# Performance work log

Hardware: AMD Instinct MI355X
Metric: run time of the kernel (lower is better)

The kernel has to match this reference:

```python
import jax, jax.numpy as jnp
import numpy as np

BETA = 1000.0   # partial_ot default beta
N_ITER = 10     # partial_ot default n_iter


def setup_inputs() -> dict:
    key = jax.random.key(0)
    k1, k2 = jax.random.split(key)
    v_emb = jax.random.normal(k1, (64, 512, 256), dtype=jnp.float32)
    a_emb = jax.random.normal(k2, (64, 512, 256), dtype=jnp.float32)
    return {"v_emb": v_emb, "a_emb": a_emb}


def reference(v_emb, a_emb):
    # calc_pot_loss of UMT with p=2: cost_routines[2](x, y) = cdist(x, y)**2 / 2.
    B, m, d = v_emb.shape
    n = a_emb.shape[1]
    # Batched squared-Euclidean cost / 2 -> [B, m, n]
    C = 0.5 * (jnp.sum(v_emb * v_emb, -1)[:, :, None]
               + jnp.sum(a_emb * a_emb, -1)[:, None, :]
               - 2.0 * jnp.einsum('bmd,bnd->bmn', v_emb, a_emb))
    T0 = jnp.exp(-C / BETA)                       # Gibbs kernel, [B, m, n]
    S0 = jnp.sum(T0, axis=(-2, -1))               # total mass, [B]
    rs0 = jnp.sum(T0[:, 0, :], axis=-1)           # row-0 sum, [B]
    cs0 = jnp.sum(T0[:, :, 0], axis=-1)           # col-0 sum, [B]

    # Literal torch semantics of partial_ot:
    #  - torch.diag(k) on the [m,1] / [n,1] vectors returns a length-1 tensor
    #    (the diagonal of an m-by-1 matrix), so T_a / T_b are SCALAR rescalings
    #    of T by min(a[0]/rowsum[0], 1) and min(b[0]/colsum[0], 1).
    #  - D is reset to +inf at the top of every s-iteration, so the returned D
    #    is exactly the value computed at the last s = min(m, n).
    # Hence every T in the s/t loops is c * T0 for a per-batch scalar c, and we
    # track only that scalar recurrence (same math, no redundant matrices).
    a0 = 1.0 / m                                  # a = ones(m,1)/m -> a[0]
    b0 = 1.0 / n                                  # b = ones(n,1)/n -> b[0]
    s = float(min(m, n))                          # only last s survives

    c = s / S0                                    # T = (s / sum(T)) * exp(-C/beta)
    for _ in range(N_ITER):
        k_a = jnp.minimum(a0 / (c * rs0), 1.0)            # diag(min(a/T@1, 1))[0]
        k_b = jnp.minimum(b0 / (k_a * c * cs0), 1.0)      # diag(min(b/T_a.T@1, 1))[0]
        c = s * k_a * k_b / S0                            # T = (s/sum(T_old)) * T_b

    D = c * jnp.einsum('bmn,bmn->b', C, T0)       # dot(C.flatten(), T.flatten())
    return jnp.mean(D)                            # mean over batch (stacked distances)
```

## Files before the change

### kernel.cpp

```cpp
#include <hip/hip_runtime.h>
#include <stdint.h>

#define BATCH 64
#define MDIM 512
#define NDIM 512
#define KDIM 256
#define BM 128
#define BN 128
#define BK 32
#define NKSTEP 8
#define NTILES 16
#define LDSW 32

typedef __attribute__((ext_vector_type(8))) short short8;
typedef __attribute__((ext_vector_type(4))) float f32x4;
typedef __attribute__((ext_vector_type(4))) unsigned int u32x4;

__device__ __forceinline__ unsigned int cvt_pk(float lo, float hi) {
  unsigned int r;
  asm("v_cvt_pk_bf16_f32 %0, %1, %2" : "=v"(r) : "v"(lo), "v"(hi));
  return r;
}

#define BARRIER()                                         \
  {                                                       \
    asm volatile("s_waitcnt lgkmcnt(0)" ::: "memory");    \
    __builtin_amdgcn_s_barrier();                         \
    asm volatile("" ::: "memory");                        \
  }

__device__ __forceinline__ float waveRedSum(float v) {
  v += __shfl_xor(v, 32);
  v += __shfl_xor(v, 16);
  v += __shfl_xor(v, 8);
  v += __shfl_xor(v, 4);
  v += __shfl_xor(v, 2);
  v += __shfl_xor(v, 1);
  return v;
}

__global__ __launch_bounds__(512, 4) void pot_gemm_reduce(
    const float* __restrict__ V, const float* __restrict__ A,
    float* __restrict__ part) {
  const int bid = blockIdx.x;
  const int lin = (bid & 7) * 128 + (bid >> 3);
  const int b   = lin >> 4;
  const int t   = lin & 15;
  const int tm  = t >> 2;
  const int tn  = t & 3;

  const int tid  = threadIdx.x;
  const int w    = tid >> 6;
  const int lane = tid & 63;
  const int wr   = w >> 2;
  const int wc   = w & 3;
  const int srow = tid >> 2;
  const int sseg = tid & 3;
  const int ssw  = (sseg ^ ((srow >> 1) & 3)) * 8;

  __shared__ short As[2][BM][LDSW];
  __shared__ short Bs[2][BN][LDSW];
  __shared__ float nvs[BM];
  __shared__ float nas[BN];
  __shared__ float red[8][4];

  const float* Vg = V + ((size_t)b * MDIM + (size_t)tm * BM + srow) * KDIM + sseg * 8;
  const float* Ag = A + ((size_t)b * NDIM + (size_t)tn * BN + srow) * KDIM + sseg * 8;

  float sqa = 0.f, sqb = 0.f;
  f32x4 acc[4][2];
#pragma unroll
  for (int m = 0; m < 4; ++m)
#pragma unroll
    for (int n = 0; n < 2; ++n)
      acc[m][n] = (f32x4){0.f, 0.f, 0.f, 0.f};

  float4 ra[2][2], rb[2][2];

#define ISSUE(k, slot)                                                        \
  {                                                                           \
    const float4* pa = reinterpret_cast<const float4*>(Vg + (k) * BK);        \
    const float4* pb = reinterpret_cast<const float4*>(Ag + (k) * BK);        \
    ra[slot][0] = pa[0]; ra[slot][1] = pa[1];                                 \
    rb[slot][0] = pb[0]; rb[slot][1] = pb[1];                                 \
  }

#define SQ4(s_, f) { s_ += (f).x*(f).x + (f).y*(f).y + (f).z*(f).z + (f).w*(f).w; }

#define WRITE(buf, slot)                                                      \
  {                                                                           \
    u32x4 wa, wb;                                                             \
    wa[0] = cvt_pk(ra[slot][0].x, ra[slot][0].y);                             \
    wa[1] = cvt_pk(ra[slot][0].z, ra[slot][0].w);                             \
    wa[2] = cvt_pk(ra[slot][1].x, ra[slot][1].y);                             \
    wa[3] = cvt_pk(ra[slot][1].z, ra[slot][1].w);                             \
    wb[0] = cvt_pk(rb[slot][0].x, rb[slot][0].y);                             \
    wb[1] = cvt_pk(rb[slot][0].z, rb[slot][0].w);                             \
    wb[2] = cvt_pk(rb[slot][1].x, rb[slot][1].y);                             \
    wb[3] = cvt_pk(rb[slot][1].z, rb[slot][1].w);                             \
    SQ4(sqa, ra[slot][0]); SQ4(sqa, ra[slot][1]);                             \
    SQ4(sqb, rb[slot][0]); SQ4(sqb, rb[slot][1]);                             \
    *reinterpret_cast<u32x4*>(&As[buf][srow][ssw]) = wa;                      \
    *reinterpret_cast<u32x4*>(&Bs[buf][srow][ssw]) = wb;                      \
  }

#define COMPUTE(buf)                                                          \
  {                                                                           \
    short8 af[4], bf[2];                                                      \
    const int fr  = lane & 15;                                                \
    const int ksw = ((lane >> 4) ^ ((fr >> 1) & 3)) * 8;   \
    _Pragma("unroll")                                                         \
    for (int m = 0; m < 4; ++m)                                               \
      af[m] = *reinterpret_cast<const short8*>(                               \
          &As[buf][wr * 64 + m * 16 + fr][ksw]);                              \
    _Pragma("unroll")                                                         \
    for (int n = 0; n < 2; ++n)                                               \
      bf[n] = *reinterpret_cast<const short8*>(                               \
          &Bs[buf][wc * 32 + n * 16 + fr][ksw]);                              \
    _Pragma("unroll")                                                         \
    for (int m = 0; m < 4; ++m)                                               \
      _Pragma("unroll")                                                       \
      for (int n = 0; n < 2; ++n)                                             \
        acc[m][n] = __builtin_amdgcn_mfma_f32_16x16x32_bf16(                  \
            af[m], bf[n], acc[m][n], 0, 0, 0);                                \
  }

  ISSUE(0, 0);
  ISSUE(1, 1);
  WRITE(0, 0);
  BARRIER();

#pragma unroll
  for (int k = 0; k < NKSTEP; ++k) {
    if (k + 2 < NKSTEP) ISSUE(k + 2, k & 1);
    COMPUTE(k & 1);
    if (k + 1 < NKSTEP) WRITE((k + 1) & 1, (k + 1) & 1);
    BARRIER();
  }

  {
    float va = sqa;
    va += __shfl_xor(va, 1); va += __shfl_xor(va, 2);
    float vb = sqb;
    vb += __shfl_xor(vb, 1); vb += __shfl_xor(vb, 2);
    if (sseg == 0) { nvs[srow] = 0.5f * va; nas[srow] = 0.5f * vb; }
  }
  BARRIER();

  float hr[4][4], hc[2];
#pragma unroll
  for (int m = 0; m < 4; ++m)
#pragma unroll
    for (int r = 0; r < 4; ++r)
      hr[m][r] = nvs[wr * 64 + m * 16 + (lane >> 4) * 4 + r];
#pragma unroll
  for (int n = 0; n < 2; ++n)
    hc[n] = nas[wc * 32 + n * 16 + (lane & 15)];

  const bool rowmask = (tm == 0) && (wr == 0) && ((lane >> 4) == 0);
  const bool colmask = (tn == 0) && (wc == 0) && ((lane & 15) == 0);
  const float k2 = -1.0e-3f * 1.4426950408889634f;

  float s0p = 0.f, ctp = 0.f, rsp = 0.f, csp = 0.f;
#pragma unroll
  for (int m = 0; m < 4; ++m) {
#pragma unroll
    for (int n = 0; n < 2; ++n) {
#pragma unroll
      for (int r = 0; r < 4; ++r) {
        float Cv = hr[m][r] + hc[n] - acc[m][n][r];
        float T = exp2f(Cv * k2);
        s0p += T;
        ctp += Cv * T;
        if (m == 0 && r == 0) rsp += rowmask ? T : 0.f;
        if (n == 0)           csp += colmask ? T : 0.f;
      }
    }
  }

  s0p = waveRedSum(s0p);
  ctp = waveRedSum(ctp);
  rsp = waveRedSum(rsp);
  csp = waveRedSum(csp);
  if (lane == 0) { red[w][0] = s0p; red[w][1] = ctp; red[w][2] = rsp; red[w][3] = csp; }
  BARRIER();
  if (tid == 0) {
    float s0 = 0.f, ct = 0.f, rs = 0.f, cs = 0.f;
#pragma unroll
    for (int i = 0; i < 8; ++i) {
      s0 += red[i][0]; ct += red[i][1]; rs += red[i][2]; cs += red[i][3];
    }
    float* p = part + ((size_t)(b * NTILES + t)) * 4;
    p[0] = s0; p[1] = ct; p[2] = rs; p[3] = cs;
  }
}

__global__ __launch_bounds__(64) void pot_finalize(
    const float* __restrict__ part, float* __restrict__ out) {
  const int b = threadIdx.x;
  float S0 = 0.f, CT = 0.f, RS = 0.f, CS = 0.f;
#pragma unroll
  for (int t = 0; t < NTILES; ++t) {
    const float* p = part + ((size_t)(b * NTILES + t)) * 4;
    S0 += p[0]; CT += p[1]; RS += p[2]; CS += p[3];
  }
  const float a0 = 1.0f / (float)MDIM;
  const float b0 = 1.0f / (float)NDIM;
  const float s  = (float)MDIM;
  float c = s / S0;
#pragma unroll
  for (int i = 0; i < 10; ++i) {
    float ka = fminf(a0 / (c * RS), 1.0f);
    float kb = fminf(b0 / (ka * c * CS), 1.0f);
    c = s * ka * kb / S0;
  }
  float D = c * CT;
  D = waveRedSum(D);
  if (b == 0) out[0] = D * (1.0f / (float)BATCH);
}

extern "C" void kernel_launch(void* const* d_in, const int* in_sizes, int n_in,
                              void* d_out, int out_size, void* d_ws, size_t ws_size,
                              hipStream_t stream) {
  const float* V = (const float*)d_in[0];
  const float* A = (const float*)d_in[1];
  float* out = (float*)d_out;
  float* part = (float*)d_ws;

  pot_gemm_reduce<<<dim3(BATCH * NTILES), 512, 0, stream>>>(V, A, part);
  pot_finalize<<<1, 64, 0, stream>>>(part, out);
}
```

Baseline: 29.96 us.

## Keep V row-tile in registers and stream all A column tiles per block

Each block now owns one 128-row V tile for one batch, loads its full K=256 slice once into LDS and then into register fragments, and loops over the four A column tiles. It double-buffers those A tiles through LDS, prefetching and converting the next tile while running MFMAs on the current one. The grid shrinks from 1024 to 256 blocks, and V is loaded and converted once instead of four times. Per-wave partials are written directly to global memory instead of being reduced in-block, so the finalize kernel reads 8x more partials. The cost is a large register footprint (afr holds 32 short8), occupancy lowered to 2 blocks per CU in the launch bounds, and a smaller grid.

```diff
diff --git a/kernel.cpp b/kernel.cpp
--- a/kernel.cpp
+++ b/kernel.cpp
@@ -3,14 +3,10 @@
 
 #define BATCH 64
 #define MDIM 512
-#define NDIM 512
 #define KDIM 256
-#define BM 128
-#define BN 128
-#define BK 32
-#define NKSTEP 8
-#define NTILES 16
-#define LDSW 32
+#define BT   128
+#define NTN  4
+#define NBLK 256
 
 typedef __attribute__((ext_vector_type(8))) short short8;
 typedef __attribute__((ext_vector_type(4))) float f32x4;
@@ -28,6 +24,8 @@
     __builtin_amdgcn_s_barrier();                         \
     asm volatile("" ::: "memory");                        \
   }
+
+#define SQ4(s_, f) { s_ += (f).x*(f).x + (f).y*(f).y + (f).z*(f).z + (f).w*(f).w; }
 
 __device__ __forceinline__ float waveRedSum(float v) {
   v += __shfl_xor(v, 32);
@@ -39,15 +37,13 @@
   return v;
 }
 
-__global__ __launch_bounds__(512, 4) void pot_gemm_reduce(
-    const float* __restrict__ V, const float* __restrict__ A,
+__global__ __launch_bounds__(512, 2) void pot_fused(
+    const float* __restrict__ V, const float* __restrict__ Ae,
     float* __restrict__ part) {
-  const int bid = blockIdx.x;
-  const int lin = (bid & 7) * 128 + (bid >> 3);
-  const int b   = lin >> 4;
-  const int t   = lin & 15;
-  const int tm  = t >> 2;
-  const int tn  = t & 3;
+  const int pid = blockIdx.x;
+  const int L   = (pid & 7) * 32 + (pid >> 3);
+  const int b   = L >> 2;
+  const int tm  = L & 3;
 
   const int tid  = threadIdx.x;
   const int w    = tid >> 6;
@@ -56,142 +52,200 @@
   const int wc   = w & 3;
   const int srow = tid >> 2;
   const int sseg = tid & 3;
-  const int ssw  = (sseg ^ ((srow >> 1) & 3)) * 8;
-
-  __shared__ short As[2][BM][LDSW];
-  __shared__ short Bs[2][BN][LDSW];
-  __shared__ float nvs[BM];
-  __shared__ float nas[BN];
-  __shared__ float red[8][4];
-
-  const float* Vg = V + ((size_t)b * MDIM + (size_t)tm * BM + srow) * KDIM + sseg * 8;
-  const float* Ag = A + ((size_t)b * NDIM + (size_t)tn * BN + srow) * KDIM + sseg * 8;
-
-  float sqa = 0.f, sqb = 0.f;
-  f32x4 acc[4][2];
-#pragma unroll
-  for (int m = 0; m < 4; ++m)
-#pragma unroll
-    for (int n = 0; n < 2; ++n)
-      acc[m][n] = (f32x4){0.f, 0.f, 0.f, 0.f};
-
-  float4 ra[2][2], rb[2][2];
-
-#define ISSUE(k, slot)                                                        \
-  {                                                                           \
-    const float4* pa = reinterpret_cast<const float4*>(Vg + (k) * BK);        \
-    const float4* pb = reinterpret_cast<const float4*>(Ag + (k) * BK);        \
-    ra[slot][0] = pa[0]; ra[slot][1] = pa[1];                                 \
-    rb[slot][0] = pb[0]; rb[slot][1] = pb[1];                                 \
-  }
-
-#define SQ4(s_, f) { s_ += (f).x*(f).x + (f).y*(f).y + (f).z*(f).z + (f).w*(f).w; }
-
-#define WRITE(buf, slot)                                                      \
-  {                                                                           \
-    u32x4 wa, wb;                                                             \
-    wa[0] = cvt_pk(ra[slot][0].x, ra[slot][0].y);                             \
-    wa[1] = cvt_pk(ra[slot][0].z, ra[slot][0].w);                             \
-    wa[2] = cvt_pk(ra[slot][1].x, ra[slot][1].y);                             \
-    wa[3] = cvt_pk(ra[slot][1].z, ra[slot][1].w);                             \
-    wb[0] = cvt_pk(rb[slot][0].x, rb[slot][0].y);                             \
-    wb[1] = cvt_pk(rb[slot][0].z, rb[slot][0].w);                             \
-    wb[2] = cvt_pk(rb[slot][1].x, rb[slot][1].y);                             \
-    wb[3] = cvt_pk(rb[slot][1].z, rb[slot][1].w);                             \
-    SQ4(sqa, ra[slot][0]); SQ4(sqa, ra[slot][1]);                             \
-    SQ4(sqb, rb[slot][0]); SQ4(sqb, rb[slot][1]);                             \
-    *reinterpret_cast<u32x4*>(&As[buf][srow][ssw]) = wa;                      \
-    *reinterpret_cast<u32x4*>(&Bs[buf][srow][ssw]) = wb;                      \
-  }
-
-#define COMPUTE(buf)                                                          \
-  {                                                                           \
-    short8 af[4], bf[2];                                                      \
-    const int fr  = lane & 15;                                                \
-    const int ksw = ((lane >> 4) ^ ((fr >> 1) & 3)) * 8;   \
-    _Pragma("unroll")                                                         \
-    for (int m = 0; m < 4; ++m)                                               \
-      af[m] = *reinterpret_cast<const short8*>(                               \
-          &As[buf][wr * 64 + m * 16 + fr][ksw]);                              \
-    _Pragma("unroll")                                                         \
-    for (int n = 0; n < 2; ++n)                                               \
-      bf[n] = *reinterpret_cast<const short8*>(                               \
-          &Bs[buf][wc * 32 + n * 16 + fr][ksw]);                              \
-    _Pragma("unroll")                                                         \
-    for (int m = 0; m < 4; ++m)                                               \
-      _Pragma("unroll")                                                       \
-      for (int n = 0; n < 2; ++n)                                             \
-        acc[m][n] = __builtin_amdgcn_mfma_f32_16x16x32_bf16(                  \
-            af[m], bf[n], acc[m][n], 0, 0, 0);                                \
-  }
-
-  ISSUE(0, 0);
-  ISSUE(1, 1);
-  WRITE(0, 0);
+  const int fr   = lane & 15;
+  const int fk   = lane >> 4;
+
+  __shared__ short buf[2][BT][KDIM];
+  __shared__ float nvs[BT];
+  __shared__ float nbs[2][BT];
+
+  const float* Arow = V  + ((size_t)b * MDIM + tm * BT + srow) * KDIM;
+  const float* Brow = Ae + ((size_t)b * MDIM + srow) * KDIM;
+
+  {
+    float4 st[16];
+#pragma unroll
+    for (int i = 0; i < 8; ++i) {
+      const float4* p = reinterpret_cast<const float4*>(Arow + (sseg + 4 * i) * 8);
+      st[2 * i] = p[0]; st[2 * i + 1] = p[1];
+    }
+    float sq = 0.f;
+#pragma unroll
+    for (int i = 0; i < 8; ++i) {
+      const int u = (sseg + 4 * i) ^ (srow & 7);
+      u32x4 wv;
+      wv[0] = cvt_pk(st[2 * i].x, st[2 * i].y);
+      wv[1] = cvt_pk(st[2 * i].z, st[2 * i].w);
+      wv[2] = cvt_pk(st[2 * i + 1].x, st[2 * i + 1].y);
+      wv[3] = cvt_pk(st[2 * i + 1].z, st[2 * i + 1].w);
+      SQ4(sq, st[2 * i]); SQ4(sq, st[2 * i + 1]);
+      *reinterpret_cast<u32x4*>(&buf[1][srow][u * 8]) = wv;
+    }
+    sq += __shfl_xor(sq, 1); sq += __shfl_xor(sq, 2);
+    if (sseg == 0) nvs[srow] = 0.5f * sq;
+  }
+
+  float4 b0st[16];
+#pragma unroll
+  for (int i = 0; i < 8; ++i) {
+    const float4* p = reinterpret_cast<const float4*>(Brow + (sseg + 4 * i) * 8);
+    b0st[2 * i] = p[0]; b0st[2 * i + 1] = p[1];
+  }
   BARRIER();
 
-#pragma unroll
-  for (int k = 0; k < NKSTEP; ++k) {
-    if (k + 2 < NKSTEP) ISSUE(k + 2, k & 1);
-    COMPUTE(k & 1);
-    if (k + 1 < NKSTEP) WRITE((k + 1) & 1, (k + 1) & 1);
+  {
+    float sq = 0.f;
+#pragma unroll
+    for (int i = 0; i < 8; ++i) {
+      const int u = (sseg + 4 * i) ^ (srow & 7);
+      u32x4 wv;
+      wv[0] = cvt_pk(b0st[2 * i].x, b0st[2 * i].y);
+      wv[1] = cvt_pk(b0st[2 * i].z, b0st[2 * i].w);
+      wv[2] = cvt_pk(b0st[2 * i + 1].x, b0st[2 * i + 1].y);
+      wv[3] = cvt_pk(b0st[2 * i + 1].z, b0st[2 * i + 1].w);
+      SQ4(sq, b0st[2 * i]); SQ4(sq, b0st[2 * i + 1]);
+      *reinterpret_cast<u32x4*>(&buf[0][srow][u * 8]) = wv;
+    }
+    sq += __shfl_xor(sq, 1); sq += __shfl_xor(sq, 2);
+    if (sseg == 0) nbs[0][srow] = 0.5f * sq;
+  }
+
+  short8 afr[4][8];
+#pragma unroll
+  for (int m = 0; m < 4; ++m) {
+#pragma unroll
+    for (int ks = 0; ks < 8; ++ks) {
+      const int row = wr * 64 + m * 16 + fr;
+      const int u   = (4 * ks + fk) ^ (row & 7);
+      afr[m][ks] = *reinterpret_cast<const short8*>(&buf[1][row][u * 8]);
+    }
+  }
+  BARRIER();
+
+  const float k2 = -1.0e-3f * 1.4426950408889634f;
+  float4 bst[2][4];
+
+#pragma unroll
+  for (int tn = 0; tn < NTN; ++tn) {
+    const int bb = tn & 1;
+    const int nb = bb ^ 1;
+    const float* Bnx = Brow + (size_t)(tn + 1) * BT * KDIM;
+
+    f32x4 acc[4][2];
+#pragma unroll
+    for (int m = 0; m < 4; ++m)
+#pragma unroll
+      for (int n = 0; n < 2; ++n)
+        acc[m][n] = (f32x4){0.f, 0.f, 0.f, 0.f};
+
+#define BISSUE(i0, slot)                                                       \
+    {                                                                          \
+      const float4* p0_ = reinterpret_cast<const float4*>(Bnx + (sseg + 4*(i0)) * 8);     \
+      const float4* p1_ = reinterpret_cast<const float4*>(Bnx + (sseg + 4*((i0)+1)) * 8); \
+      bst[slot][0] = p0_[0]; bst[slot][1] = p0_[1];                            \
+      bst[slot][2] = p1_[0]; bst[slot][3] = p1_[1];                            \
+    }
+#define BWRITE(i0, slot)                                                       \
+    {                                                                          \
+      int u_ = (sseg + 4*(i0)) ^ (srow & 7);                                   \
+      u32x4 wv_;                                                               \
+      wv_[0] = cvt_pk(bst[slot][0].x, bst[slot][0].y);                         \
+      wv_[1] = cvt_pk(bst[slot][0].z, bst[slot][0].w);                         \
+      wv_[2] = cvt_pk(bst[slot][1].x, bst[slot][1].y);                         \
+      wv_[3] = cvt_pk(bst[slot][1].z, bst[slot][1].w);                         \
+      SQ4(sqb, bst[slot][0]); SQ4(sqb, bst[slot][1]);                          \
+      *reinterpret_cast<u32x4*>(&buf[nb][srow][u_ * 8]) = wv_;                 \
+      u_ = (sseg + 4*((i0)+1)) ^ (srow & 7);                                   \
+      wv_[0] = cvt_pk(bst[slot][2].x, bst[slot][2].y);                         \
+      wv_[1] = cvt_pk(bst[slot][2].z, bst[slot][2].w);                         \
+      wv_[2] = cvt_pk(bst[slot][3].x, bst[slot][3].y);                         \
+      wv_[3] = cvt_pk(bst[slot][3].z, bst[slot][3].w);                         \
+      SQ4(sqb, bst[slot][2]); SQ4(sqb, bst[slot][3]);                          \
+      *reinterpret_cast<u32x4*>(&buf[nb][srow][u_ * 8]) = wv_;                 \
+    }
+
+    float sqb = 0.f;
+    short8 bfr[2][2];
+#pragma unroll
+    for (int n = 0; n < 2; ++n) {
+      const int row = wc * 32 + n * 16 + fr;
+      const int u   = fk ^ (row & 7);
+      bfr[0][n] = *reinterpret_cast<const short8*>(&buf[bb][row][u * 8]);
+    }
+
+#pragma unroll
+    for (int ks = 0; ks < 8; ++ks) {
+      if (ks < 7) {
+#pragma unroll
+        for (int n = 0; n < 2; ++n) {
+          const int row = wc * 32 + n * 16 + fr;
+          const int u   = (4 * (ks + 1) + fk) ^ (row & 7);
+          bfr[(ks + 1) & 1][n] =
+              *reinterpret_cast<const short8*>(&buf[bb][row][u * 8]);
+        }
+      }
+      if (tn < NTN - 1) {
+        if (ks == 0) { BISSUE(0, 0); }
+        if (ks == 2) { BWRITE(0, 0); BISSUE(2, 1); }
+        if (ks == 4) { BWRITE(2, 1); BISSUE(4, 0); }
+        if (ks == 6) { BWRITE(4, 0); BISSUE(6, 1); }
+      }
+#pragma unroll
+      for (int m = 0; m < 4; ++m)
+#pragma unroll
+        for (int n = 0; n < 2; ++n)
+          acc[m][n] = __builtin_amdgcn_mfma_f32_16x16x32_bf16(
+              afr[m][ks], bfr[ks & 1][n], acc[m][n], 0, 0, 0);
+    }
+
+    if (tn < NTN - 1) {
+      BWRITE(6, 1);
+      sqb += __shfl_xor(sqb, 1); sqb += __shfl_xor(sqb, 2);
+      if (sseg == 0) nbs[nb][srow] = 0.5f * sqb;
+    }
+
+    {
+      float hr[4][4], hc[2];
+#pragma unroll
+      for (int m = 0; m < 4; ++m)
+#pragma unroll
+        for (int r = 0; r < 4; ++r)
+          hr[m][r] = nvs[wr * 64 + m * 16 + fk * 4 + r];
+#pragma unroll
+      for (int n = 0; n < 2; ++n)
+        hc[n] = nbs[bb][wc * 32 + n * 16 + fr];
+
+      const bool rowmask = (tm == 0) && (wr == 0) && (fk == 0);
+      const bool colmask = (tn == 0) && (wc == 0) && (fr == 0);
+
+      float s0p = 0.f, ctp = 0.f, rsp = 0.f, csp = 0.f;
+#pragma unroll
+      for (int m = 0; m < 4; ++m) {
+#pragma unroll
+        for (int n = 0; n < 2; ++n) {
+#pragma unroll
+          for (int r = 0; r < 4; ++r) {
+            float Cv = hr[m][r] + hc[n] - acc[m][n][r];
+            float T = exp2f(Cv * k2);
+            s0p += T;
+            ctp += Cv * T;
+            if (m == 0 && r == 0) rsp += rowmask ? T : 0.f;
+            if (n == 0)           csp += colmask ? T : 0.f;
+          }
+        }
+      }
+      s0p = waveRedSum(s0p);
+      ctp = waveRedSum(ctp);
+      rsp = waveRedSum(rsp);
+      csp = waveRedSum(csp);
+      if (lane == 0) {
+        float* p = part + (((size_t)(L * NTN + tn)) * 8 + w) * 4;
+        p[0] = s0p; p[1] = ctp; p[2] = rsp; p[3] = csp;
+      }
+    }
     BARRIER();
-  }
-
-  {
-    float va = sqa;
-    va += __shfl_xor(va, 1); va += __shfl_xor(va, 2);
-    float vb = sqb;
-    vb += __shfl_xor(vb, 1); vb += __shfl_xor(vb, 2);
-    if (sseg == 0) { nvs[srow] = 0.5f * va; nas[srow] = 0.5f * vb; }
-  }
-  BARRIER();
-
-  float hr[4][4], hc[2];
-#pragma unroll
-  for (int m = 0; m < 4; ++m)
-#pragma unroll
-    for (int r = 0; r < 4; ++r)
-      hr[m][r] = nvs[wr * 64 + m * 16 + (lane >> 4) * 4 + r];
-#pragma unroll
-  for (int n = 0; n < 2; ++n)
-    hc[n] = nas[wc * 32 + n * 16 + (lane & 15)];
-
-  const bool rowmask = (tm == 0) && (wr == 0) && ((lane >> 4) == 0);
-  const bool colmask = (tn == 0) && (wc == 0) && ((lane & 15) == 0);
-  const float k2 = -1.0e-3f * 1.4426950408889634f;
-
-  float s0p = 0.f, ctp = 0.f, rsp = 0.f, csp = 0.f;
-#pragma unroll
-  for (int m = 0; m < 4; ++m) {
-#pragma unroll
-    for (int n = 0; n < 2; ++n) {
-#pragma unroll
-      for (int r = 0; r < 4; ++r) {
-        float Cv = hr[m][r] + hc[n] - acc[m][n][r];
-        float T = exp2f(Cv * k2);
-        s0p += T;
-        ctp += Cv * T;
-        if (m == 0 && r == 0) rsp += rowmask ? T : 0.f;
-        if (n == 0)           csp += colmask ? T : 0.f;
-      }
-    }
-  }
-
-  s0p = waveRedSum(s0p);
-  ctp = waveRedSum(ctp);
-  rsp = waveRedSum(rsp);
-  csp = waveRedSum(csp);
-  if (lane == 0) { red[w][0] = s0p; red[w][1] = ctp; red[w][2] = rsp; red[w][3] = csp; }
-  BARRIER();
-  if (tid == 0) {
-    float s0 = 0.f, ct = 0.f, rs = 0.f, cs = 0.f;
-#pragma unroll
-    for (int i = 0; i < 8; ++i) {
-      s0 += red[i][0]; ct += red[i][1]; rs += red[i][2]; cs += red[i][3];
-    }
-    float* p = part + ((size_t)(b * NTILES + t)) * 4;
-    p[0] = s0; p[1] = ct; p[2] = rs; p[3] = cs;
+#undef BISSUE
+#undef BWRITE
   }
 }
 
@@ -200,12 +254,18 @@
   const int b = threadIdx.x;
   float S0 = 0.f, CT = 0.f, RS = 0.f, CS = 0.f;
 #pragma unroll
-  for (int t = 0; t < NTILES; ++t) {
-    const float* p = part + ((size_t)(b * NTILES + t)) * 4;
-    S0 += p[0]; CT += p[1]; RS += p[2]; CS += p[3];
+  for (int tm = 0; tm < 4; ++tm) {
+    const int L = 4 * b + tm;
+#pragma unroll
+    for (int tn = 0; tn < NTN; ++tn) {
+      for (int wv = 0; wv < 8; ++wv) {
+        const float* p = part + (((size_t)(L * NTN + tn)) * 8 + wv) * 4;
+        S0 += p[0]; CT += p[1]; RS += p[2]; CS += p[3];
+      }
+    }
   }
   const float a0 = 1.0f / (float)MDIM;
-  const float b0 = 1.0f / (float)NDIM;
+  const float b0 = 1.0f / (float)MDIM;
   const float s  = (float)MDIM;
   float c = s / S0;
 #pragma unroll
@@ -222,11 +282,11 @@
 extern "C" void kernel_launch(void* const* d_in, const int* in_sizes, int n_in,
                               void* d_out, int out_size, void* d_ws, size_t ws_size,
                               hipStream_t stream) {
-  const float* V = (const float*)d_in[0];
-  const float* A = (const float*)d_in[1];
-  float* out = (float*)d_out;
+  const float* V  = (const float*)d_in[0];
+  const float* Ae = (const float*)d_in[1];
+  float* out  = (float*)d_out;
   float* part = (float*)d_ws;
 
-  pot_gemm_reduce<<<dim3(BATCH * NTILES), 512, 0, stream>>>(V, A, part);
+  pot_fused<<<dim3(NBLK), 512, 0, stream>>>(V, Ae, part);
   pot_finalize<<<1, 64, 0, stream>>>(part, out);
 }
```

New measurement: 36.74 us. 22.6% more time.

## Restructure GEMM tiles: full-K A strip in LDS, B fed straight from registers

Applied to the files above, without the earlier changes.

Each block now loads a 64-row strip of V with the full K depth into LDS once and computes 64x256 output tiles. Each wave streams its own 32 columns of A from global memory straight into MFMA B-operand registers, with no LDS staging or per-step barriers. Per-wave partial sums are written directly, which removes the block-level reduction, and the finalize kernel is widened to 256 threads. The aim is to cut barrier and LDS traffic and raise occupancy. The cost is no software prefetch on the global loads for A and more partials to reduce at the end.

```diff
diff --git a/kernel.cpp b/kernel.cpp
--- a/kernel.cpp
+++ b/kernel.cpp
@@ -3,14 +3,10 @@
 
 #define BATCH 64
 #define MDIM 512
-#define NDIM 512
 #define KDIM 256
-#define BM 128
-#define BN 128
-#define BK 32
-#define NKSTEP 8
-#define NTILES 16
-#define LDSW 32
+#define ROWS 64
+#define HCOLS 256
+#define NBLK 1024
 
 typedef __attribute__((ext_vector_type(8))) short short8;
 typedef __attribute__((ext_vector_type(4))) float f32x4;
@@ -21,13 +17,6 @@
   asm("v_cvt_pk_bf16_f32 %0, %1, %2" : "=v"(r) : "v"(lo), "v"(hi));
   return r;
 }
-
-#define BARRIER()                                         \
-  {                                                       \
-    asm volatile("s_waitcnt lgkmcnt(0)" ::: "memory");    \
-    __builtin_amdgcn_s_barrier();                         \
-    asm volatile("" ::: "memory");                        \
-  }
 
 __device__ __forceinline__ float waveRedSum(float v) {
   v += __shfl_xor(v, 32);
@@ -39,126 +28,109 @@
   return v;
 }
 
-__global__ __launch_bounds__(512, 4) void pot_gemm_reduce(
-    const float* __restrict__ V, const float* __restrict__ A,
+__global__ __launch_bounds__(512, 8) void pot_gemm_reduce(
+    const float* __restrict__ V, const float* __restrict__ Ae,
     float* __restrict__ part) {
   const int bid = blockIdx.x;
   const int lin = (bid & 7) * 128 + (bid >> 3);
-  const int b   = lin >> 4;
-  const int t   = lin & 15;
-  const int tm  = t >> 2;
-  const int tn  = t & 3;
+  const int b     = lin >> 4;
+  const int strip = (lin >> 1) & 7;
+  const int half  = lin & 1;
 
   const int tid  = threadIdx.x;
   const int w    = tid >> 6;
   const int lane = tid & 63;
-  const int wr   = w >> 2;
-  const int wc   = w & 3;
-  const int srow = tid >> 2;
-  const int sseg = tid & 3;
-  const int ssw  = (sseg ^ ((srow >> 1) & 3)) * 8;
-
-  __shared__ short As[2][BM][LDSW];
-  __shared__ short Bs[2][BN][LDSW];
-  __shared__ float nvs[BM];
-  __shared__ float nas[BN];
-  __shared__ float red[8][4];
-
-  const float* Vg = V + ((size_t)b * MDIM + (size_t)tm * BM + srow) * KDIM + sseg * 8;
-  const float* Ag = A + ((size_t)b * NDIM + (size_t)tn * BN + srow) * KDIM + sseg * 8;
-
-  float sqa = 0.f, sqb = 0.f;
+  const int fr   = lane & 15;
+  const int fk   = lane >> 4;
+  const int frl  = fr & 7;
+
+  __shared__ short As[ROWS][KDIM];
+  __shared__ float nvs[ROWS];
+
+  {
+    const int row = tid >> 3;
+    const int j   = tid & 7;
+    const float* Ar = V + ((size_t)b * MDIM + strip * ROWS + row) * KDIM;
+    float sq = 0.f;
+#pragma unroll
+    for (int i = 0; i < 4; ++i) {
+      const int u = j * 4 + i;
+      const float4* p = reinterpret_cast<const float4*>(Ar + u * 8);
+      float4 x = p[0], y = p[1];
+      u32x4 wv;
+      wv[0] = cvt_pk(x.x, x.y); wv[1] = cvt_pk(x.z, x.w);
+      wv[2] = cvt_pk(y.x, y.y); wv[3] = cvt_pk(y.z, y.w);
+      sq += x.x * x.x + x.y * x.y + x.z * x.z + x.w * x.w;
+      sq += y.x * y.x + y.y * y.y + y.z * y.z + y.w * y.w;
+      *reinterpret_cast<u32x4*>(&As[row][(u ^ (row & 7)) * 8]) = wv;
+    }
+    sq += __shfl_xor(sq, 1);
+    sq += __shfl_xor(sq, 2);
+    sq += __shfl_xor(sq, 4);
+    if (j == 0) nvs[row] = 0.5f * sq;
+  }
+  __syncthreads();
+
+  const int gcb = half * HCOLS + w * 32;
+  const float* B0 = Ae + ((size_t)b * MDIM + gcb + fr) * KDIM + fk * 8;
+  const float* B1 = B0 + 16 * KDIM;
+
   f32x4 acc[4][2];
 #pragma unroll
   for (int m = 0; m < 4; ++m)
 #pragma unroll
     for (int n = 0; n < 2; ++n)
       acc[m][n] = (f32x4){0.f, 0.f, 0.f, 0.f};
-
-  float4 ra[2][2], rb[2][2];
-
-#define ISSUE(k, slot)                                                        \
-  {                                                                           \
-    const float4* pa = reinterpret_cast<const float4*>(Vg + (k) * BK);        \
-    const float4* pb = reinterpret_cast<const float4*>(Ag + (k) * BK);        \
-    ra[slot][0] = pa[0]; ra[slot][1] = pa[1];                                 \
-    rb[slot][0] = pb[0]; rb[slot][1] = pb[1];                                 \
-  }
-
-#define SQ4(s_, f) { s_ += (f).x*(f).x + (f).y*(f).y + (f).z*(f).z + (f).w*(f).w; }
-
-#define WRITE(buf, slot)                                                      \
-  {                                                                           \
-    u32x4 wa, wb;                                                             \
-    wa[0] = cvt_pk(ra[slot][0].x, ra[slot][0].y);                             \
-    wa[1] = cvt_pk(ra[slot][0].z, ra[slot][0].w);                             \
-    wa[2] = cvt_pk(ra[slot][1].x, ra[slot][1].y);                             \
-    wa[3] = cvt_pk(ra[slot][1].z, ra[slot][1].w);                             \
-    wb[0] = cvt_pk(rb[slot][0].x, rb[slot][0].y);                             \
-    wb[1] = cvt_pk(rb[slot][0].z, rb[slot][0].w);                             \
-    wb[2] = cvt_pk(rb[slot][1].x, rb[slot][1].y);                             \
-    wb[3] = cvt_pk(rb[slot][1].z, rb[slot][1].w);                             \
-    SQ4(sqa, ra[slot][0]); SQ4(sqa, ra[slot][1]);                             \
-    SQ4(sqb, rb[slot][0]); SQ4(sqb, rb[slot][1]);                             \
-    *reinterpret_cast<u32x4*>(&As[buf][srow][ssw]) = wa;                      \
-    *reinterpret_cast<u32x4*>(&Bs[buf][srow][ssw]) = wb;                      \
-  }
-
-#define COMPUTE(buf)                                                          \
-  {                                                                           \
-    short8 af[4], bf[2];                                                      \
-    const int fr  = lane & 15;                                                \
-    const int ksw = ((lane >> 4) ^ ((fr >> 1) & 3)) * 8;   \
-    _Pragma("unroll")                                                         \
-    for (int m = 0; m < 4; ++m)                                               \
-      af[m] = *reinterpret_cast<const short8*>(                               \
-          &As[buf][wr * 64 + m * 16 + fr][ksw]);                              \
-    _Pragma("unroll")                                                         \
-    for (int n = 0; n < 2; ++n)                                               \
-      bf[n] = *reinterpret_cast<const short8*>(                               \
-          &Bs[buf][wc * 32 + n * 16 + fr][ksw]);                              \
-    _Pragma("unroll")                                                         \
-    for (int m = 0; m < 4; ++m)                                               \
-      _Pragma("unroll")                                                       \
-      for (int n = 0; n < 2; ++n)                                             \
-        acc[m][n] = __builtin_amdgcn_mfma_f32_16x16x32_bf16(                  \
-            af[m], bf[n], acc[m][n], 0, 0, 0);                                \
-  }
-
-  ISSUE(0, 0);
-  ISSUE(1, 1);
-  WRITE(0, 0);
-  BARRIER();
-
-#pragma unroll
-  for (int k = 0; k < NKSTEP; ++k) {
-    if (k + 2 < NKSTEP) ISSUE(k + 2, k & 1);
-    COMPUTE(k & 1);
-    if (k + 1 < NKSTEP) WRITE((k + 1) & 1, (k + 1) & 1);
-    BARRIER();
-  }
-
-  {
-    float va = sqa;
-    va += __shfl_xor(va, 1); va += __shfl_xor(va, 2);
-    float vb = sqb;
-    vb += __shfl_xor(vb, 1); vb += __shfl_xor(vb, 2);
-    if (sseg == 0) { nvs[srow] = 0.5f * va; nas[srow] = 0.5f * vb; }
-  }
-  BARRIER();
-
-  float hr[4][4], hc[2];
+  float sqb0 = 0.f, sqb1 = 0.f;
+
+#pragma unroll
+  for (int ks = 0; ks < 8; ++ks) {
+    float4 x0 = *reinterpret_cast<const float4*>(B0 + ks * 32);
+    float4 x1 = *reinterpret_cast<const float4*>(B0 + ks * 32 + 4);
+    float4 y0 = *reinterpret_cast<const float4*>(B1 + ks * 32);
+    float4 y1 = *reinterpret_cast<const float4*>(B1 + ks * 32 + 4);
+    u32x4 t0, t1;
+    t0[0] = cvt_pk(x0.x, x0.y); t0[1] = cvt_pk(x0.z, x0.w);
+    t0[2] = cvt_pk(x1.x, x1.y); t0[3] = cvt_pk(x1.z, x1.w);
+    t1[0] = cvt_pk(y0.x, y0.y); t1[1] = cvt_pk(y0.z, y0.w);
+    t1[2] = cvt_pk(y1.x, y1.y); t1[3] = cvt_pk(y1.z, y1.w);
+    sqb0 += x0.x * x0.x + x0.y * x0.y + x0.z * x0.z + x0.w * x0.w;
+    sqb0 += x1.x * x1.x + x1.y * x1.y + x1.z * x1.z + x1.w * x1.w;
+    sqb1 += y0.x * y0.x + y0.y * y0.y + y0.z * y0.z + y0.w * y0.w;
+    sqb1 += y1.x * y1.x + y1.y * y1.y + y1.z * y1.z + y1.w * y1.w;
+    short8 bf0 = *reinterpret_cast<short8*>(&t0);
+    short8 bf1 = *reinterpret_cast<short8*>(&t1);
+
+    const int su = ((4 * ks + fk) ^ frl) * 8;
+    short8 af0 = *reinterpret_cast<const short8*>(&As[fr][su]);
+    short8 af1 = *reinterpret_cast<const short8*>(&As[16 + fr][su]);
+    short8 af2 = *reinterpret_cast<const short8*>(&As[32 + fr][su]);
+    short8 af3 = *reinterpret_cast<const short8*>(&As[48 + fr][su]);
+
+    acc[0][0] = __builtin_amdgcn_mfma_f32_16x16x32_bf16(af0, bf0, acc[0][0], 0, 0, 0);
+    acc[0][1] = __builtin_amdgcn_mfma_f32_16x16x32_bf16(af0, bf1, acc[0][1], 0, 0, 0);
+    acc[1][0] = __builtin_amdgcn_mfma_f32_16x16x32_bf16(af1, bf0, acc[1][0], 0, 0, 0);
+    acc[1][1] = __builtin_amdgcn_mfma_f32_16x16x32_bf16(af1, bf1, acc[1][1], 0, 0, 0);
+    acc[2][0] = __builtin_amdgcn_mfma_f32_16x16x32_bf16(af2, bf0, acc[2][0], 0, 0, 0);
+    acc[2][1] = __builtin_amdgcn_mfma_f32_16x16x32_bf16(af2, bf1, acc[2][1], 0, 0, 0);
+    acc[3][0] = __builtin_amdgcn_mfma_f32_16x16x32_bf16(af3, bf0, acc[3][0], 0, 0, 0);
+    acc[3][1] = __builtin_amdgcn_mfma_f32_16x16x32_bf16(af3, bf1, acc[3][1], 0, 0, 0);
+  }
+
+  sqb0 += __shfl_xor(sqb0, 16); sqb0 += __shfl_xor(sqb0, 32);
+  sqb1 += __shfl_xor(sqb1, 16); sqb1 += __shfl_xor(sqb1, 32);
+  const float hc0 = 0.5f * sqb0;
+  const float hc1 = 0.5f * sqb1;
+
+  float hr[4][4];
 #pragma unroll
   for (int m = 0; m < 4; ++m)
 #pragma unroll
     for (int r = 0; r < 4; ++r)
-      hr[m][r] = nvs[wr * 64 + m * 16 + (lane >> 4) * 4 + r];
-#pragma unroll
-  for (int n = 0; n < 2; ++n)
-    hc[n] = nas[wc * 32 + n * 16 + (lane & 15)];
-
-  const bool rowmask = (tm == 0) && (wr == 0) && ((lane >> 4) == 0);
-  const bool colmask = (tn == 0) && (wc == 0) && ((lane & 15) == 0);
+      hr[m][r] = nvs[m * 16 + fk * 4 + r];
+
+  const bool rowmask = (strip == 0) && (fk == 0);
+  const bool colmask = (half == 0) && (w == 0) && (fr == 0);
   const float k2 = -1.0e-3f * 1.4426950408889634f;
 
   float s0p = 0.f, ctp = 0.f, rsp = 0.f, csp = 0.f;
@@ -168,7 +140,7 @@
     for (int n = 0; n < 2; ++n) {
 #pragma unroll
       for (int r = 0; r < 4; ++r) {
-        float Cv = hr[m][r] + hc[n] - acc[m][n][r];
+        float Cv = hr[m][r] + (n ? hc1 : hc0) - acc[m][n][r];
         float T = exp2f(Cv * k2);
         s0p += T;
         ctp += Cv * T;
@@ -182,51 +154,59 @@
   ctp = waveRedSum(ctp);
   rsp = waveRedSum(rsp);
   csp = waveRedSum(csp);
-  if (lane == 0) { red[w][0] = s0p; red[w][1] = ctp; red[w][2] = rsp; red[w][3] = csp; }
-  BARRIER();
-  if (tid == 0) {
-    float s0 = 0.f, ct = 0.f, rs = 0.f, cs = 0.f;
-#pragma unroll
-    for (int i = 0; i < 8; ++i) {
-      s0 += red[i][0]; ct += red[i][1]; rs += red[i][2]; cs += red[i][3];
+  if (lane == 0) {
+    float* p = part + (((size_t)((b * 16 + strip * 2 + half)) * 8 + w)) * 4;
+    p[0] = s0p; p[1] = ctp; p[2] = rsp; p[3] = csp;
+  }
+}
+
+__global__ __launch_bounds__(256) void pot_finalize(
+    const float* __restrict__ part, float* __restrict__ out) {
+  __shared__ float dred[BATCH];
+  const int t = threadIdx.x;
+  const int batch = t >> 2;
+  const int q = t & 3;
+
+  float S0 = 0.f, CT = 0.f, RS = 0.f, CS = 0.f;
+  const f32x4* p4 = reinterpret_cast<const f32x4*>(part);
+#pragma unroll
+  for (int i = 0; i < 32; ++i) {
+    f32x4 v = p4[batch * 128 + q * 32 + i];
+    S0 += v[0]; CT += v[1]; RS += v[2]; CS += v[3];
+  }
+  S0 += __shfl_xor(S0, 1); S0 += __shfl_xor(S0, 2);
+  CT += __shfl_xor(CT, 1); CT += __shfl_xor(CT, 2);
+  RS += __shfl_xor(RS, 1); RS += __shfl_xor(RS, 2);
+  CS += __shfl_xor(CS, 1); CS += __shfl_xor(CS, 2);
+
+  if (q == 0) {
+    const float a0 = 1.0f / (float)MDIM;
+    const float b0 = 1.0f / (float)MDIM;
+    const float s  = (float)MDIM;
+    float c = s / S0;
+#pragma unroll
+    for (int i = 0; i < 10; ++i) {
+      float ka = fminf(a0 / (c * RS), 1.0f);
+      float kb = fminf(b0 / (ka * c * CS), 1.0f);
+      c = s * ka * kb / S0;
     }
-    float* p = part + ((size_t)(b * NTILES + t)) * 4;
-    p[0] = s0; p[1] = ct; p[2] = rs; p[3] = cs;
-  }
-}
-
-__global__ __launch_bounds__(64) void pot_finalize(
-    const float* __restrict__ part, float* __restrict__ out) {
-  const int b = threadIdx.x;
-  float S0 = 0.f, CT = 0.f, RS = 0.f, CS = 0.f;
-#pragma unroll
-  for (int t = 0; t < NTILES; ++t) {
-    const float* p = part + ((size_t)(b * NTILES + t)) * 4;
-    S0 += p[0]; CT += p[1]; RS += p[2]; CS += p[3];
-  }
-  const float a0 = 1.0f / (float)MDIM;
-  const float b0 = 1.0f / (float)NDIM;
-  const float s  = (float)MDIM;
-  float c = s / S0;
-#pragma unroll
-  for (int i = 0; i < 10; ++i) {
-    float ka = fminf(a0 / (c * RS), 1.0f);
-    float kb = fminf(b0 / (ka * c * CS), 1.0f);
-    c = s * ka * kb / S0;
-  }
-  float D = c * CT;
-  D = waveRedSum(D);
-  if (b == 0) out[0] = D * (1.0f / (float)BATCH);
+    dred[batch] = c * CT;
+  }
+  __syncthreads();
+  if (t < 64) {
+    float D = waveRedSum(dred[t]);
+    if (t == 0) out[0] = D * (1.0f / (float)BATCH);
+  }
 }
 
 extern "C" void kernel_launch(void* const* d_in, const int* in_sizes, int n_in,
                               void* d_out, int out_size, void* d_ws, size_t ws_size,
                               hipStream_t stream) {
-  const float* V = (const float*)d_in[0];
-  const float* A = (const float*)d_in[1];
-  float* out = (float*)d_out;
+  const float* V  = (const float*)d_in[0];
+  const float* Ae = (const float*)d_in[1];
+  float* out  = (float*)d_out;
   float* part = (float*)d_ws;
 
-  pot_gemm_reduce<<<dim3(BATCH * NTILES), 512, 0, stream>>>(V, A, part);
-  pot_finalize<<<1, 64, 0, stream>>>(part, out);
-}
+  pot_gemm_reduce<<<dim3(NBLK), 512, 0, stream>>>(V, Ae, part);
+  pot_finalize<<<1, 256, 0, stream>>>(part, out);
+}
```

After: 78.95 us. 164% more time.

## Shrink GEMM tile to 128x64 with 256-thread blocks and single-stage prefetch

Applied to the files above, without the earlier changes.

Halves the N tile to 64 so the grid grows to 2048 blocks of 256 threads (4 waves), with launch bounds raised to 5 blocks per CU. The global-load prefetch depth drops from two register slots to one, which saves registers. The load mapping is reworked so each thread loads 16 floats of A and 8 of B. The goal is more blocks and better occupancy and wave balance across CUs. The cost is more reloading of V across N tiles and less latency hiding per block.

```diff
diff --git a/kernel.cpp b/kernel.cpp
--- a/kernel.cpp
+++ b/kernel.cpp
@@ -3,14 +3,15 @@
 
 #define BATCH 64
 #define MDIM 512
-#define NDIM 512
 #define KDIM 256
 #define BM 128
-#define BN 128
+#define BN 64
 #define BK 32
 #define NKSTEP 8
-#define NTILES 16
-#define LDSW 32
+#define TILES_M 4
+#define TILES_N 8
+#define NTILES 32
+#define NBLK 2048
 
 typedef __attribute__((ext_vector_type(8))) short short8;
 typedef __attribute__((ext_vector_type(4))) float f32x4;
@@ -28,6 +29,8 @@
     __builtin_amdgcn_s_barrier();                         \
     asm volatile("" ::: "memory");                        \
   }
+
+#define SQ4(s_, f) { s_ += (f).x*(f).x + (f).y*(f).y + (f).z*(f).z + (f).w*(f).w; }
 
 __device__ __forceinline__ float waveRedSum(float v) {
   v += __shfl_xor(v, 32);
@@ -39,33 +42,37 @@
   return v;
 }
 
-__global__ __launch_bounds__(512, 4) void pot_gemm_reduce(
-    const float* __restrict__ V, const float* __restrict__ A,
+__global__ __launch_bounds__(256, 5) void pot_gemm_reduce(
+    const float* __restrict__ V, const float* __restrict__ Ae,
     float* __restrict__ part) {
   const int bid = blockIdx.x;
-  const int lin = (bid & 7) * 128 + (bid >> 3);
-  const int b   = lin >> 4;
-  const int t   = lin & 15;
-  const int tm  = t >> 2;
-  const int tn  = t & 3;
+  const int lin = (bid & 7) * 256 + (bid >> 3);
+  const int b   = lin >> 5;
+  const int t   = lin & 31;
+  const int tm  = t >> 3;
+  const int tn  = t & 7;
 
   const int tid  = threadIdx.x;
   const int w    = tid >> 6;
   const int lane = tid & 63;
-  const int wr   = w >> 2;
-  const int wc   = w & 3;
-  const int srow = tid >> 2;
-  const int sseg = tid & 3;
-  const int ssw  = (sseg ^ ((srow >> 1) & 3)) * 8;
-
-  __shared__ short As[2][BM][LDSW];
-  __shared__ short Bs[2][BN][LDSW];
+  const int wr   = w >> 1;
+  const int wc   = w & 1;
+  const int fr   = lane & 15;
+  const int fk   = lane >> 4;
+
+  const int arow  = tid >> 1;
+  const int ahalf = tid & 1;
+  const int brow  = tid >> 2;
+  const int bunit = tid & 3;
+
+  __shared__ short As[2][BM][BK];
+  __shared__ short Bs[2][BN][BK];
   __shared__ float nvs[BM];
-  __shared__ float nas[BN];
-  __shared__ float red[8][4];
-
-  const float* Vg = V + ((size_t)b * MDIM + (size_t)tm * BM + srow) * KDIM + sseg * 8;
-  const float* Ag = A + ((size_t)b * NDIM + (size_t)tn * BN + srow) * KDIM + sseg * 8;
+  __shared__ float nbs[BN];
+  __shared__ float red[4][4];
+
+  const float* Vg = V  + ((size_t)b * MDIM + tm * BM + arow) * KDIM + ahalf * 16;
+  const float* Bg = Ae + ((size_t)b * MDIM + tn * BN + brow) * KDIM + bunit * 8;
 
   float sqa = 0.f, sqb = 0.f;
   f32x4 acc[4][2];
@@ -75,48 +82,47 @@
     for (int n = 0; n < 2; ++n)
       acc[m][n] = (f32x4){0.f, 0.f, 0.f, 0.f};
 
-  float4 ra[2][2], rb[2][2];
-
-#define ISSUE(k, slot)                                                        \
+  float4 ra0, ra1, ra2, ra3, rb0, rb1;
+
+#define ISSUE(k)                                                              \
   {                                                                           \
     const float4* pa = reinterpret_cast<const float4*>(Vg + (k) * BK);        \
-    const float4* pb = reinterpret_cast<const float4*>(Ag + (k) * BK);        \
-    ra[slot][0] = pa[0]; ra[slot][1] = pa[1];                                 \
-    rb[slot][0] = pb[0]; rb[slot][1] = pb[1];                                 \
-  }
-
-#define SQ4(s_, f) { s_ += (f).x*(f).x + (f).y*(f).y + (f).z*(f).z + (f).w*(f).w; }
-
-#define WRITE(buf, slot)                                                      \
+    const float4* pb = reinterpret_cast<const float4*>(Bg + (k) * BK);        \
+    ra0 = pa[0]; ra1 = pa[1]; ra2 = pa[2]; ra3 = pa[3];                       \
+    rb0 = pb[0]; rb1 = pb[1];                                                 \
+  }
+
+#define WRITE(buf)                                                            \
   {                                                                           \
-    u32x4 wa, wb;                                                             \
-    wa[0] = cvt_pk(ra[slot][0].x, ra[slot][0].y);                             \
-    wa[1] = cvt_pk(ra[slot][0].z, ra[slot][0].w);                             \
-    wa[2] = cvt_pk(ra[slot][1].x, ra[slot][1].y);                             \
-    wa[3] = cvt_pk(ra[slot][1].z, ra[slot][1].w);                             \
-    wb[0] = cvt_pk(rb[slot][0].x, rb[slot][0].y);                             \
-    wb[1] = cvt_pk(rb[slot][0].z, rb[slot][0].w);                             \
-    wb[2] = cvt_pk(rb[slot][1].x, rb[slot][1].y);                             \
-    wb[3] = cvt_pk(rb[slot][1].z, rb[slot][1].w);                             \
-    SQ4(sqa, ra[slot][0]); SQ4(sqa, ra[slot][1]);                             \
-    SQ4(sqb, rb[slot][0]); SQ4(sqb, rb[slot][1]);                             \
-    *reinterpret_cast<u32x4*>(&As[buf][srow][ssw]) = wa;                      \
-    *reinterpret_cast<u32x4*>(&Bs[buf][srow][ssw]) = wb;                      \
+    u32x4 wa0, wa1, wb;                                                       \
+    wa0[0] = cvt_pk(ra0.x, ra0.y); wa0[1] = cvt_pk(ra0.z, ra0.w);             \
+    wa0[2] = cvt_pk(ra1.x, ra1.y); wa0[3] = cvt_pk(ra1.z, ra1.w);             \
+    wa1[0] = cvt_pk(ra2.x, ra2.y); wa1[1] = cvt_pk(ra2.z, ra2.w);             \
+    wa1[2] = cvt_pk(ra3.x, ra3.y); wa1[3] = cvt_pk(ra3.z, ra3.w);             \
+    wb[0]  = cvt_pk(rb0.x, rb0.y); wb[1]  = cvt_pk(rb0.z, rb0.w);             \
+    wb[2]  = cvt_pk(rb1.x, rb1.y); wb[3]  = cvt_pk(rb1.z, rb1.w);             \
+    SQ4(sqa, ra0); SQ4(sqa, ra1); SQ4(sqa, ra2); SQ4(sqa, ra3);               \
+    SQ4(sqb, rb0); SQ4(sqb, rb1);                                             \
+    const int au0 = (ahalf * 2 + 0) ^ ((arow >> 1) & 3);                      \
+    const int au1 = (ahalf * 2 + 1) ^ ((arow >> 1) & 3);                      \
+    const int bu  = bunit ^ ((brow >> 1) & 3);                                \
+    *reinterpret_cast<u32x4*>(&As[buf][arow][au0 * 8]) = wa0;                 \
+    *reinterpret_cast<u32x4*>(&As[buf][arow][au1 * 8]) = wa1;                 \
+    *reinterpret_cast<u32x4*>(&Bs[buf][brow][bu * 8])  = wb;                  \
   }
 
 #define COMPUTE(buf)                                                          \
   {                                                                           \
     short8 af[4], bf[2];                                                      \
-    const int fr  = lane & 15;                                                \
-    const int ksw = ((lane >> 4) ^ ((fr >> 1) & 3)) * 8;   \
+    const int ru = (fk ^ ((fr >> 1) & 3)) * 8;                                \
     _Pragma("unroll")                                                         \
     for (int m = 0; m < 4; ++m)                                               \
       af[m] = *reinterpret_cast<const short8*>(                               \
-          &As[buf][wr * 64 + m * 16 + fr][ksw]);                              \
+          &As[buf][wr * 64 + m * 16 + fr][ru]);                               \
     _Pragma("unroll")                                                         \
     for (int n = 0; n < 2; ++n)                                               \
       bf[n] = *reinterpret_cast<const short8*>(                               \
-          &Bs[buf][wc * 32 + n * 16 + fr][ksw]);                              \
+          &Bs[buf][wc * 32 + n * 16 + fr][ru]);                               \
     _Pragma("unroll")                                                         \
     for (int m = 0; m < 4; ++m)                                               \
       _Pragma("unroll")                                                       \
@@ -125,25 +131,24 @@
             af[m], bf[n], acc[m][n], 0, 0, 0);                                \
   }
 
-  ISSUE(0, 0);
-  ISSUE(1, 1);
-  WRITE(0, 0);
+  ISSUE(0);
+  WRITE(0);
   BARRIER();
 
 #pragma unroll
   for (int k = 0; k < NKSTEP; ++k) {
-    if (k + 2 < NKSTEP) ISSUE(k + 2, k & 1);
+    if (k + 1 < NKSTEP) ISSUE(k + 1);
     COMPUTE(k & 1);
-    if (k + 1 < NKSTEP) WRITE((k + 1) & 1, (k + 1) & 1);
+    if (k + 1 < NKSTEP) WRITE((k + 1) & 1);
     BARRIER();
   }
 
   {
-    float va = sqa;
-    va += __shfl_xor(va, 1); va += __shfl_xor(va, 2);
+    float va = sqa + __shfl_xor(sqa, 1);
+    if (ahalf == 0) nvs[arow] = 0.5f * va;
     float vb = sqb;
     vb += __shfl_xor(vb, 1); vb += __shfl_xor(vb, 2);
-    if (sseg == 0) { nvs[srow] = 0.5f * va; nas[srow] = 0.5f * vb; }
+    if (bunit == 0) nbs[brow] = 0.5f * vb;
   }
   BARRIER();
 
@@ -152,13 +157,13 @@
   for (int m = 0; m < 4; ++m)
 #pragma unroll
     for (int r = 0; r < 4; ++r)
-      hr[m][r] = nvs[wr * 64 + m * 16 + (lane >> 4) * 4 + r];
+      hr[m][r] = nvs[wr * 64 + m * 16 + fk * 4 + r];
 #pragma unroll
   for (int n = 0; n < 2; ++n)
-    hc[n] = nas[wc * 32 + n * 16 + (lane & 15)];
-
-  const bool rowmask = (tm == 0) && (wr == 0) && ((lane >> 4) == 0);
-  const bool colmask = (tn == 0) && (wc == 0) && ((lane & 15) == 0);
+    hc[n] = nbs[wc * 32 + n * 16 + fr];
+
+  const bool rowmask = (tm == 0) && (wr == 0) && (fk == 0);
+  const bool colmask = (tn == 0) && (wc == 0) && (fr == 0);
   const float k2 = -1.0e-3f * 1.4426950408889634f;
 
   float s0p = 0.f, ctp = 0.f, rsp = 0.f, csp = 0.f;
@@ -183,11 +188,11 @@
   rsp = waveRedSum(rsp);
   csp = waveRedSum(csp);
   if (lane == 0) { red[w][0] = s0p; red[w][1] = ctp; red[w][2] = rsp; red[w][3] = csp; }
-  BARRIER();
+  __syncthreads();
   if (tid == 0) {
     float s0 = 0.f, ct = 0.f, rs = 0.f, cs = 0.f;
 #pragma unroll
-    for (int i = 0; i < 8; ++i) {
+    for (int i = 0; i < 4; ++i) {
       s0 += red[i][0]; ct += red[i][1]; rs += red[i][2]; cs += red[i][3];
     }
     float* p = part + ((size_t)(b * NTILES + t)) * 4;
@@ -205,7 +210,7 @@
     S0 += p[0]; CT += p[1]; RS += p[2]; CS += p[3];
   }
   const float a0 = 1.0f / (float)MDIM;
-  const float b0 = 1.0f / (float)NDIM;
+  const float b0 = 1.0f / (float)MDIM;
   const float s  = (float)MDIM;
   float c = s / S0;
 #pragma unroll
@@ -222,11 +227,11 @@
 extern "C" void kernel_launch(void* const* d_in, const int* in_sizes, int n_in,
                               void* d_out, int out_size, void* d_ws, size_t ws_size,
                               hipStream_t stream) {
-  const float* V = (const float*)d_in[0];
-  const float* A = (const float*)d_in[1];
-  float* out = (float*)d_out;
+  const float* V  = (const float*)d_in[0];
+  const float* Ae = (const float*)d_in[1];
+  float* out  = (float*)d_out;
   float* part = (float*)d_ws;
 
-  pot_gemm_reduce<<<dim3(BATCH * NTILES), 512, 0, stream>>>(V, A, part);
+  pot_gemm_reduce<<<dim3(NBLK), 256, 0, stream>>>(V, Ae, part);
   pot_finalize<<<1, 64, 0, stream>>>(part, out);
 }
```

Measured after the change: 68.17 us. 2.28x slower.
